# Optimization experiments

Measured on AMD Instinct MI355X. Metric: run time of the kernel, lower is better.

The kernel has to match this reference:

```python
import jax, jax.numpy as jnp
import numpy as np

B, N, EMB = 8, 1024, 768
HEADS = 8
INNER = EMB // HEADS          # 96: qkv inner dim (per the module's unusual design)
HEAD_D = INNER // HEADS       # 12: per-head dim after 'b n (h d) -> b h n d'
MLP = 3072
EPS = 1e-5


def _layernorm(x, g, b):
    mu = jnp.mean(x, axis=-1, keepdims=True)
    var = jnp.mean(jnp.square(x - mu), axis=-1, keepdims=True)
    return (x - mu) * jax.lax.rsqrt(var + EPS) * g + b


def setup_inputs() -> dict:
    key = jax.random.key(0)
    ks = jax.random.split(key, 8)
    s = 0.02
    return {
        "inputs": jax.random.normal(ks[0], (B, N, EMB), jnp.float32),
        "behaviors": jax.random.normal(ks[1], (B, 3), jnp.float32),
        "mouse_id": 0,
        "ln1_g": jnp.ones((EMB,), jnp.float32),
        "ln1_b": jnp.zeros((EMB,), jnp.float32),
        "w_qkv": jax.random.normal(ks[2], (EMB, 3 * INNER), jnp.float32) * s,
        "w_proj": jax.random.normal(ks[3], (INNER, EMB), jnp.float32) * s,
        "b_proj": jnp.zeros((EMB,), jnp.float32),
        "ln2_g": jnp.ones((EMB,), jnp.float32),
        "ln2_b": jnp.zeros((EMB,), jnp.float32),
        "w1": jax.random.normal(ks[4], (EMB, MLP), jnp.float32) * s,
        "b1": jnp.zeros((MLP,), jnp.float32),
        "w2": jax.random.normal(ks[5], (MLP, EMB), jnp.float32) * s,
        "b2": jnp.zeros((EMB,), jnp.float32),
    }


def reference(inputs, behaviors, mouse_id, ln1_g, ln1_b, w_qkv, w_proj, b_proj,
              ln2_g, ln2_b, w1, b1, w2, b2):
    # behavior_mode=0 -> b_mlp is None; dropout/drop_path = 0 -> identity.
    x = inputs
    # --- Attention (pre-LN) ---
    h = _layernorm(x, ln1_g, ln1_b)
    qkv = h @ w_qkv                                   # [B, N, 3*INNER]
    q, k, v = jnp.split(qkv, 3, axis=-1)
    def split_heads(a):
        return a.reshape(B, N, HEADS, HEAD_D)         # b n h d
    q = split_heads(q) * (INNER ** -0.5)              # scale = inner_dim^-0.5 (as in source)
    k = split_heads(k)
    v = split_heads(v)
    attn = jax.nn.softmax(jnp.einsum("bihd,bjhd->bhij", q, k), axis=-1)
    out = jnp.einsum("bhij,bjhd->bihd", attn, v).reshape(B, N, INNER)
    x = x + (out @ w_proj + b_proj)
    # --- MLP (pre-LN) ---
    m = _layernorm(x, ln2_g, ln2_b)
    m = jax.nn.gelu(m @ w1 + b1, approximate=False)   # nn.GELU default = exact erf
    x = x + (m @ w2 + b2)
    return x
```

## Files before the change

### kernel.cpp

```cpp
#include <hip/hip_runtime.h>
#include <hip/hip_bf16.h>
#include <math.h>

#define BB 8
#define NSEQ 1024
#define EMB 768
#define HEADS 8
#define INNER 96
#define HEAD_D 12
#define MLP_DIM 3072
#define ROWS (BB * NSEQ)

using short8  = __attribute__((ext_vector_type(8))) short;
using s4b     = __attribute__((ext_vector_type(4))) short;
using floatx4 = __attribute__((ext_vector_type(4))) float;

#define GLL16(g, l)                                                          \
    __builtin_amdgcn_global_load_lds(                                        \
        (const __attribute__((address_space(1))) void*)(g),                  \
        (__attribute__((address_space(3))) void*)(l), 16, 0, 0)

static __device__ __forceinline__ ushort f2b(float x) {
    __hip_bfloat16 h = __float2bfloat16(x);
    return *reinterpret_cast<ushort*>(&h);
}
static __device__ __forceinline__ uint pk2(float a, float b) {
    return (uint)f2b(a) | ((uint)f2b(b) << 16);
}

static __device__ __forceinline__ floatx4 mfma16(s4b a, s4b b, floatx4 c) {
#if __has_builtin(__builtin_amdgcn_mfma_f32_16x16x16_bf16)
    return __builtin_amdgcn_mfma_f32_16x16x16_bf16(a, b, c, 0, 0, 0);
#elif __has_builtin(__builtin_amdgcn_mfma_f32_16x16x16bf16_1k)
    return __builtin_amdgcn_mfma_f32_16x16x16bf16_1k(a, b, c, 0, 0, 0);
#else
    floatx4 d;
    asm("v_mfma_f32_16x16x16_bf16 %0, %1, %2, %3" : "=v"(d) : "v"(a), "v"(b), "v"(c));
    return d;
#endif
}

__global__ __launch_bounds__(256) void ln_bf16_kernel(const float* __restrict__ x,
                                                      const float* __restrict__ g,
                                                      const float* __restrict__ b,
                                                      ushort* __restrict__ out) {
    int row  = blockIdx.x * 4 + (threadIdx.x >> 6);
    int lane = threadIdx.x & 63;
    const float* xr = x + (size_t)row * EMB;
    float v[12];
    float s = 0.f;
#pragma unroll
    for (int i = 0; i < 12; i++) {
        v[i] = xr[lane + i * 64];
        s += v[i];
    }
#pragma unroll
    for (int off = 32; off; off >>= 1) s += __shfl_xor(s, off);
    float mu = s * (1.0f / EMB);
    float ss = 0.f;
#pragma unroll
    for (int i = 0; i < 12; i++) { float d = v[i] - mu; ss += d * d; }
#pragma unroll
    for (int off = 32; off; off >>= 1) ss += __shfl_xor(ss, off);
    float rstd = rsqrtf(ss * (1.0f / EMB) + 1e-5f);
    ushort* orow = out + (size_t)row * EMB;
#pragma unroll
    for (int i = 0; i < 12; i++) {
        int c = lane + i * 64;
        orow[c] = f2b((v[i] - mu) * rstd * g[c] + b[c]);
    }
}

__global__ __launch_bounds__(256) void convt_kernel(const float* __restrict__ in,
                                                    ushort* __restrict__ out,
                                                    int K, int N, int Npad) {
    __shared__ float t[32][33];
    int n0 = blockIdx.x * 32, k0 = blockIdx.y * 32;
    int tx = threadIdx.x, ty = threadIdx.y;
#pragma unroll
    for (int i = 0; i < 32; i += 8) {
        int n = n0 + tx;
        t[ty + i][tx] = (n < N) ? in[(size_t)(k0 + ty + i) * N + n] : 0.f;
    }
    __syncthreads();
#pragma unroll
    for (int i = 0; i < 32; i += 8) {
        out[(size_t)(n0 + ty + i) * K + k0 + tx] = f2b(t[tx][ty + i]);
    }
}

__global__ __launch_bounds__(256) void convt_pad_kernel(const float* __restrict__ in,
                                                        ushort* __restrict__ out,
                                                        int K, int N, int Kpad) {
    __shared__ float t[32][33];
    int n0 = blockIdx.x * 32, k0 = blockIdx.y * 32;
    int tx = threadIdx.x, ty = threadIdx.y;
#pragma unroll
    for (int i = 0; i < 32; i += 8) {
        int k = k0 + ty + i;
        t[ty + i][tx] = (k < K) ? in[(size_t)k * N + n0 + tx] : 0.f;
    }
    __syncthreads();
#pragma unroll
    for (int i = 0; i < 32; i += 8) {
        out[(size_t)(n0 + ty + i) * Kpad + k0 + tx] = f2b(t[tx][ty + i]);
    }
}

template <int EPI, bool MASKN>
__global__ __launch_bounds__(256) void gemm_mfma(const ushort* __restrict__ A,
                                                 const ushort* __restrict__ Bt,
                                                 void* __restrict__ Cout,
                                                 const float* __restrict__ bias,
                                                 const float* __restrict__ res,
                                                 int M, int Nn, int K, int gx) {
    __shared__ ushort As[2][128 * 64];
    __shared__ ushort Bs[2][128 * 64];
    int tid  = threadIdx.x;
    int lane = tid & 63, wave = tid >> 6;
    int wm = wave >> 1, wn = wave & 1;

    int nwg = gridDim.x;
    int lin = blockIdx.x;
    int swz = (lin & 7) * (nwg >> 3) + (lin >> 3);
    int by = swz / gx, bx = swz - by * gx;
    int m0 = by * 128, n0 = bx * 128;

    floatx4 acc[4][4] = {};

    int srow = lane >> 3;
    int slot = lane & 7;
    int nt = K >> 6;

    auto STAGE = [&](int t, int bufi) {
        int k0 = t << 6;
#pragma unroll
        for (int r = 0; r < 4; r++) {
            int row = r * 32 + wave * 8 + srow;
            int c   = slot ^ (row & 7);
            const ushort* ga = A  + (size_t)(m0 + row) * K + k0 + c * 8;
            const ushort* gb = Bt + (size_t)(n0 + row) * K + k0 + c * 8;
            GLL16(ga, (char*)&As[bufi][0] + r * 4096 + wave * 1024);
            GLL16(gb, (char*)&Bs[bufi][0] + r * 4096 + wave * 1024);
        }
    };

    STAGE(0, 0);
    STAGE(1, 1);
    asm volatile("s_waitcnt vmcnt(8)" ::: "memory");
    __builtin_amdgcn_s_barrier();
    __builtin_amdgcn_sched_barrier(0);

    int cur = 0;
    for (int t = 0; t < nt; ++t) {
        short8 af[2][4], bfr[2][4];
#pragma unroll
        for (int ks = 0; ks < 2; ks++) {
#pragma unroll
            for (int mi = 0; mi < 4; mi++) {
                int row = wm * 64 + mi * 16 + (lane & 15);
                int c   = ks * 4 + (lane >> 4);
                af[ks][mi] = *(const short8*)(&As[cur][0] + row * 64 + (c ^ (row & 7)) * 8);
            }
#pragma unroll
            for (int ni = 0; ni < 4; ni++) {
                int col = wn * 64 + ni * 16 + (lane & 15);
                int c   = ks * 4 + (lane >> 4);
                bfr[ks][ni] = *(const short8*)(&Bs[cur][0] + col * 64 + (c ^ (col & 7)) * 8);
            }
        }
        asm volatile("s_waitcnt lgkmcnt(0)" ::: "memory");
        __builtin_amdgcn_s_barrier();
        __builtin_amdgcn_sched_barrier(0);

        int tn = t + 2; if (tn > nt - 1) tn = nt - 1;
        STAGE(tn, cur);

        asm volatile("s_waitcnt vmcnt(8)" ::: "memory");
        __builtin_amdgcn_sched_barrier(0);

#pragma unroll
        for (int ks = 0; ks < 2; ks++)
#pragma unroll
            for (int mi = 0; mi < 4; mi++)
#pragma unroll
                for (int ni = 0; ni < 4; ni++)
                    acc[mi][ni] = __builtin_amdgcn_mfma_f32_16x16x32_bf16(
                        af[ks][mi], bfr[ks][ni], acc[mi][ni], 0, 0, 0);

        __builtin_amdgcn_s_barrier();
        __builtin_amdgcn_sched_barrier(0);
        cur ^= 1;
    }

    int r0 = m0 + wm * 64 + (lane >> 4) * 4;
    int c0 = n0 + wn * 64 + (lane & 15);
#pragma unroll
    for (int mi = 0; mi < 4; mi++) {
#pragma unroll
        for (int ni = 0; ni < 4; ni++) {
            int col = c0 + ni * 16;
            if (MASKN && col >= Nn) continue;
#pragma unroll
            for (int r = 0; r < 4; r++) {
                int row = r0 + mi * 16 + r;
                size_t idx = (size_t)row * Nn + col;
                float v = acc[mi][ni][r];
                if constexpr (EPI == 0) {
                    ((float*)Cout)[idx] = v;
                } else if constexpr (EPI == 1) {
                    ((float*)Cout)[idx] = v + bias[col] + res[idx];
                } else {
                    v += bias[col];
                    float u = v * (1.0f + 0.044715f * v * v);
                    float gl = v / (1.0f + __expf(-1.5957691216057308f * u));
                    ((ushort*)Cout)[idx] = f2b(gl);
                }
            }
        }
    }
}

__global__ __launch_bounds__(256) void attn_mfma_kernel(const float* __restrict__ qkv,
                                                        ushort* __restrict__ ao) {
    __shared__ ushort Kt[NSEQ * 12];
    __shared__ ushort VT[12 * 1032];
    int bh = blockIdx.x >> 3, qg = blockIdx.x & 7;
    int b = bh >> 3, h = bh & 7;
    int tid = threadIdx.x;
    const float* base = qkv + (size_t)b * NSEQ * (3 * INNER);

#pragma unroll
    for (int i = 0; i < 4; i++) {
        int j = i * 256 + tid;
        const float* kp = base + (size_t)j * (3 * INNER) + INNER + h * HEAD_D;
        float4 a0 = *(const float4*)(kp);
        float4 a1 = *(const float4*)(kp + 4);
        float4 a2 = *(const float4*)(kp + 8);
        uint2* kw = (uint2*)(&Kt[j * 12]);
        kw[0] = make_uint2(pk2(a0.x, a0.y), pk2(a0.z, a0.w));
        kw[1] = make_uint2(pk2(a1.x, a1.y), pk2(a1.z, a1.w));
        kw[2] = make_uint2(pk2(a2.x, a2.y), pk2(a2.z, a2.w));
        const float* vp = kp + INNER;
        float4 v0 = *(const float4*)(vp);
        float4 v1 = *(const float4*)(vp + 4);
        float4 v2 = *(const float4*)(vp + 8);
        VT[0 * 1032 + j] = f2b(v0.x);  VT[1 * 1032 + j]  = f2b(v0.y);
        VT[2 * 1032 + j] = f2b(v0.z);  VT[3 * 1032 + j]  = f2b(v0.w);
        VT[4 * 1032 + j] = f2b(v1.x);  VT[5 * 1032 + j]  = f2b(v1.y);
        VT[6 * 1032 + j] = f2b(v1.z);  VT[7 * 1032 + j]  = f2b(v1.w);
        VT[8 * 1032 + j] = f2b(v2.x);  VT[9 * 1032 + j]  = f2b(v2.y);
        VT[10 * 1032 + j] = f2b(v2.z); VT[11 * 1032 + j] = f2b(v2.w);
    }
    __syncthreads();

    int lane = tid & 63, wave = tid >> 6;
    int qrow = lane & 15, grp = lane >> 4;
    const float scale = 0.102062072615966f;

    s4b qf[2];
#pragma unroll
    for (int t = 0; t < 2; t++) {
        qf[t] = (s4b)0;
        if (grp < 3) {
            int q = qg * 128 + (wave * 2 + t) * 16 + qrow;
            const float* qp = base + (size_t)q * (3 * INNER) + h * HEAD_D + grp * 4;
            float4 qv = *(const float4*)(qp);
            uint2 u = make_uint2(pk2(qv.x * scale, qv.y * scale),
                                 pk2(qv.z * scale, qv.w * scale));
            qf[t] = __builtin_bit_cast(s4b, u);
        }
    }

    floatx4 acc[2] = {};
    float l[2] = {0.f, 0.f};
    int kc = (grp < 3) ? grp : 0;
    int dv = (qrow < 12) ? qrow : 0;
    bool kz = (grp == 3), vz = (qrow >= 12);
    const floatx4 z4 = {};

    for (int jt = 0; jt < 64; jt++) {
        s4b kf = *(const s4b*)(&Kt[(jt * 16 + qrow) * 12 + kc * 4]);
        if (kz) kf = (s4b)0;
        s4b vf = *(const s4b*)(&VT[dv * 1032 + jt * 16 + grp * 4]);
        if (vz) vf = (s4b)0;
#pragma unroll
        for (int t = 0; t < 2; t++) {
            floatx4 st = mfma16(kf, qf[t], z4);
            float p0 = __expf(st[0]), p1 = __expf(st[1]);
            float p2 = __expf(st[2]), p3 = __expf(st[3]);
            l[t] += (p0 + p1) + (p2 + p3);
            uint2 u = make_uint2(pk2(p0, p1), pk2(p2, p3));
            acc[t] = mfma16(vf, __builtin_bit_cast(s4b, u), acc[t]);
        }
    }

#pragma unroll
    for (int t = 0; t < 2; t++) {
        float lt = l[t];
        lt += __shfl_xor(lt, 16);
        lt += __shfl_xor(lt, 32);
        float inv = 1.f / lt;
        if (grp < 3) {
            int q = qg * 128 + (wave * 2 + t) * 16 + qrow;
            ushort4 o;
            o.x = f2b(acc[t][0] * inv);
            o.y = f2b(acc[t][1] * inv);
            o.z = f2b(acc[t][2] * inv);
            o.w = f2b(acc[t][3] * inv);
            *reinterpret_cast<ushort4*>(&ao[(size_t)(b * NSEQ + q) * 128 + h * HEAD_D + grp * 4]) = o;
        }
    }
}

extern "C" void kernel_launch(void* const* d_in, const int* in_sizes, int n_in,
                              void* d_out, int out_size, void* d_ws, size_t ws_size,
                              hipStream_t stream) {
    const float* inputs = (const float*)d_in[0];
    const float* ln1_g  = (const float*)d_in[3];
    const float* ln1_b  = (const float*)d_in[4];
    const float* w_qkv  = (const float*)d_in[5];
    const float* w_proj = (const float*)d_in[6];
    const float* b_proj = (const float*)d_in[7];
    const float* ln2_g  = (const float*)d_in[8];
    const float* ln2_b  = (const float*)d_in[9];
    const float* w1     = (const float*)d_in[10];
    const float* b1     = (const float*)d_in[11];
    const float* w2     = (const float*)d_in[12];
    const float* b2     = (const float*)d_in[13];
    float* out = (float*)d_out;

    char* ws = (char*)d_ws;
    ushort* h_bf    = (ushort*)(ws);
    float*  qkv     = (float*)(ws + 12582912);
    ushort* ao_pad  = (ushort*)(ws + 22020096);
    ushort* wproj_t = (ushort*)(ws + 24117248);
    float*  x1      = (float*)(ws + 25165824);
    ushort* m2      = (ushort*)(ws + 50331648);
    ushort* wqkv_t  = (ushort*)(ws + 100663296);
    ushort* w1_t    = (ushort*)(ws + 101253120);
    ushort* w2_t    = (ushort*)(ws + 105971712);

    dim3 tb(32, 8);
    convt_kernel<<<dim3(12, 24), tb, 0, stream>>>(w_qkv, wqkv_t, EMB, 3 * INNER, 384);
    convt_kernel<<<dim3(96, 24), tb, 0, stream>>>(w1, w1_t, EMB, MLP_DIM, MLP_DIM);
    convt_kernel<<<dim3(24, 96), tb, 0, stream>>>(w2, w2_t, MLP_DIM, EMB, EMB);
    convt_pad_kernel<<<dim3(24, 4), tb, 0, stream>>>(w_proj, wproj_t, INNER, EMB, 128);

    ln_bf16_kernel<<<ROWS / 4, 256, 0, stream>>>(inputs, ln1_g, ln1_b, h_bf);
    gemm_mfma<0, true><<<3 * (ROWS / 128), 256, 0, stream>>>(
        h_bf, wqkv_t, qkv, nullptr, nullptr, ROWS, 3 * INNER, EMB, 3);
    hipMemsetAsync(ao_pad, 0, (size_t)ROWS * 128 * 2, stream);
    attn_mfma_kernel<<<512, 256, 0, stream>>>(qkv, ao_pad);
    gemm_mfma<1, false><<<6 * (ROWS / 128), 256, 0, stream>>>(
        ao_pad, wproj_t, x1, b_proj, inputs, ROWS, EMB, 128, 6);
    ln_bf16_kernel<<<ROWS / 4, 256, 0, stream>>>(x1, ln2_g, ln2_b, h_bf);
    gemm_mfma<2, false><<<24 * (ROWS / 128), 256, 0, stream>>>(
        h_bf, w1_t, m2, b1, nullptr, ROWS, MLP_DIM, EMB, 24);
    gemm_mfma<1, false><<<6 * (ROWS / 128), 256, 0, stream>>>(
        m2, w2_t, out, b2, x1, ROWS, EMB, MLP_DIM, 6);
}
```

Measured before the change: 192.5 us.

## Use 256x128 tiles with 8 waves and triple-buffered LDS pipeline in GEMM

Replaces the 4-wave 128x128 double-buffered GEMM with an 8-wave 256x128 tile kernel that uses three LDS stages. Global-to-LDS loads for tile t+2 are split across two half-steps so they interleave with the MFMA bursts, and s_setprio is raised around those bursts. LDS addresses are precomputed once outside the loop. The aim is better latency hiding and more B-tile reuse per block. The cost is higher LDS use per block (about 144KB), which limits occupancy, and fewer blocks for the small-N GEMMs; the QKV GEMM launches only 96 blocks.

```diff
diff --git a/kernel.cpp b/kernel.cpp
--- a/kernel.cpp
+++ b/kernel.cpp
@@ -39,6 +39,7 @@
     return d;
 #endif
 }
+#define MFMA32(a, b, c) __builtin_amdgcn_mfma_f32_16x16x32_bf16((a), (b), (c), 0, 0, 0)
 
 __global__ __launch_bounds__(256) void ln_bf16_kernel(const float* __restrict__ x,
                                                       const float* __restrict__ g,
@@ -108,93 +109,155 @@
 }
 
 template <int EPI, bool MASKN>
-__global__ __launch_bounds__(256) void gemm_mfma(const ushort* __restrict__ A,
-                                                 const ushort* __restrict__ Bt,
-                                                 void* __restrict__ Cout,
-                                                 const float* __restrict__ bias,
-                                                 const float* __restrict__ res,
-                                                 int M, int Nn, int K, int gx) {
-    __shared__ ushort As[2][128 * 64];
-    __shared__ ushort Bs[2][128 * 64];
-    int tid  = threadIdx.x;
-    int lane = tid & 63, wave = tid >> 6;
-    int wm = wave >> 1, wn = wave & 1;
-
-    int nwg = gridDim.x;
-    int lin = blockIdx.x;
+__global__ __launch_bounds__(512) void gemm_mfma8(const ushort* __restrict__ A,
+                                                  const ushort* __restrict__ Bt,
+                                                  void* __restrict__ Cout,
+                                                  const float* __restrict__ bias,
+                                                  const float* __restrict__ res,
+                                                  int M, int Nn, int K, int gx) {
+    __shared__ ushort As3[3][256 * 64];
+    __shared__ ushort Bs3[3][128 * 64];
+    int tid = threadIdx.x, lane = tid & 63, w = tid >> 6;
+    int wm = w >> 1, wn = w & 1;
+
+    int nwg = gridDim.x, lin = blockIdx.x;
     int swz = (lin & 7) * (nwg >> 3) + (lin >> 3);
     int by = swz / gx, bx = swz - by * gx;
-    int m0 = by * 128, n0 = bx * 128;
+    int m0 = by * 256, n0 = bx * 128;
+    int nt = K >> 6;
+
+    int srow = lane >> 3;
+    int kchunk = (lane & 7) ^ srow;
+    const ushort* gA[4];
+    const ushort* gB[2];
+    uint loAB[4];
+#pragma unroll
+    for (int s = 0; s < 4; s++) {
+        int r = s * 64 + w * 8 + srow;
+        gA[s] = A + (size_t)(m0 + r) * K + kchunk * 8;
+        loAB[s] = (uint)(s * 512 + w * 64) * 16;
+    }
+#pragma unroll
+    for (int s = 0; s < 2; s++) {
+        int r = s * 64 + w * 8 + srow;
+        gB[s] = Bt + (size_t)(n0 + r) * K + kchunk * 8;
+    }
+#define STG_A(s_, buf_, kt_) GLL16(gA[s_] + (kt_) * 64, (char*)&As3[buf_][0] + loAB[s_])
+#define STG_B(s_, buf_, kt_) GLL16(gB[s_] + (kt_) * 64, (char*)&Bs3[buf_][0] + loAB[s_])
+
+    int qr = lane & 15, grp = lane >> 4;
+    uint aoff[2][4], boff[2][4];
+#pragma unroll
+    for (int ks = 0; ks < 2; ks++) {
+#pragma unroll
+        for (int mi = 0; mi < 4; mi++) {
+            int r = wm * 64 + mi * 16 + qr;
+            aoff[ks][mi] = (uint)(r * 64 + (((ks * 4 + grp) ^ (r & 7)) * 8));
+        }
+#pragma unroll
+        for (int ni = 0; ni < 4; ni++) {
+            int c = wn * 64 + ni * 16 + qr;
+            boff[ks][ni] = (uint)(c * 64 + (((ks * 4 + grp) ^ (c & 7)) * 8));
+        }
+    }
+
+    STG_A(0, 0, 0); STG_A(1, 0, 0); STG_A(2, 0, 0); STG_A(3, 0, 0);
+    STG_B(0, 0, 0); STG_B(1, 0, 0);
+    STG_A(0, 1, 1); STG_A(1, 1, 1); STG_A(2, 1, 1); STG_A(3, 1, 1);
+    STG_B(0, 1, 1); STG_B(1, 1, 1);
+    asm volatile("s_waitcnt vmcnt(6)" ::: "memory");
+    __builtin_amdgcn_sched_barrier(0);
+    __builtin_amdgcn_s_barrier();
 
     floatx4 acc[4][4] = {};
 
-    int srow = lane >> 3;
-    int slot = lane & 7;
-    int nt = K >> 6;
-
-    auto STAGE = [&](int t, int bufi) {
-        int k0 = t << 6;
-#pragma unroll
-        for (int r = 0; r < 4; r++) {
-            int row = r * 32 + wave * 8 + srow;
-            int c   = slot ^ (row & 7);
-            const ushort* ga = A  + (size_t)(m0 + row) * K + k0 + c * 8;
-            const ushort* gb = Bt + (size_t)(n0 + row) * K + k0 + c * 8;
-            GLL16(ga, (char*)&As[bufi][0] + r * 4096 + wave * 1024);
-            GLL16(gb, (char*)&Bs[bufi][0] + r * 4096 + wave * 1024);
-        }
-    };
-
-    STAGE(0, 0);
-    STAGE(1, 1);
-    asm volatile("s_waitcnt vmcnt(8)" ::: "memory");
-    __builtin_amdgcn_s_barrier();
-    __builtin_amdgcn_sched_barrier(0);
-
-    int cur = 0;
     for (int t = 0; t < nt; ++t) {
-        short8 af[2][4], bfr[2][4];
-#pragma unroll
-        for (int ks = 0; ks < 2; ks++) {
-#pragma unroll
-            for (int mi = 0; mi < 4; mi++) {
-                int row = wm * 64 + mi * 16 + (lane & 15);
-                int c   = ks * 4 + (lane >> 4);
-                af[ks][mi] = *(const short8*)(&As[cur][0] + row * 64 + (c ^ (row & 7)) * 8);
+        int buf = t % 3;
+        int nbuf = buf + 2; if (nbuf >= 3) nbuf -= 3;
+        const ushort* Ab = &As3[buf][0];
+        const ushort* Bb = &Bs3[buf][0];
+        bool st = (t + 2) < nt;
+        int t2 = t + 2;
+
+        {
+            short8 av0 = *(const short8*)(Ab + aoff[0][0]);
+            short8 av1 = *(const short8*)(Ab + aoff[0][1]);
+            short8 av2 = *(const short8*)(Ab + aoff[0][2]);
+            short8 av3 = *(const short8*)(Ab + aoff[0][3]);
+            short8 bv0 = *(const short8*)(Bb + boff[0][0]);
+            short8 bv1 = *(const short8*)(Bb + boff[0][1]);
+            short8 bv2 = *(const short8*)(Bb + boff[0][2]);
+            short8 bv3 = *(const short8*)(Bb + boff[0][3]);
+            if (st) { STG_A(0, nbuf, t2); STG_A(1, nbuf, t2); STG_A(2, nbuf, t2); }
+            __builtin_amdgcn_s_barrier();
+            asm volatile("s_waitcnt lgkmcnt(0)" ::: "memory");
+            __builtin_amdgcn_sched_barrier(0);
+            __builtin_amdgcn_s_setprio(1);
+            acc[0][0] = MFMA32(av0, bv0, acc[0][0]);
+            acc[0][1] = MFMA32(av0, bv1, acc[0][1]);
+            acc[0][2] = MFMA32(av0, bv2, acc[0][2]);
+            acc[0][3] = MFMA32(av0, bv3, acc[0][3]);
+            acc[1][0] = MFMA32(av1, bv0, acc[1][0]);
+            acc[1][1] = MFMA32(av1, bv1, acc[1][1]);
+            acc[1][2] = MFMA32(av1, bv2, acc[1][2]);
+            acc[1][3] = MFMA32(av1, bv3, acc[1][3]);
+            acc[2][0] = MFMA32(av2, bv0, acc[2][0]);
+            acc[2][1] = MFMA32(av2, bv1, acc[2][1]);
+            acc[2][2] = MFMA32(av2, bv2, acc[2][2]);
+            acc[2][3] = MFMA32(av2, bv3, acc[2][3]);
+            acc[3][0] = MFMA32(av3, bv0, acc[3][0]);
+            acc[3][1] = MFMA32(av3, bv1, acc[3][1]);
+            acc[3][2] = MFMA32(av3, bv2, acc[3][2]);
+            acc[3][3] = MFMA32(av3, bv3, acc[3][3]);
+            __builtin_amdgcn_s_setprio(0);
+            __builtin_amdgcn_sched_barrier(0);
+            __builtin_amdgcn_s_barrier();
+        }
+        {
+            short8 av0 = *(const short8*)(Ab + aoff[1][0]);
+            short8 av1 = *(const short8*)(Ab + aoff[1][1]);
+            short8 av2 = *(const short8*)(Ab + aoff[1][2]);
+            short8 av3 = *(const short8*)(Ab + aoff[1][3]);
+            short8 bv0 = *(const short8*)(Bb + boff[1][0]);
+            short8 bv1 = *(const short8*)(Bb + boff[1][1]);
+            short8 bv2 = *(const short8*)(Bb + boff[1][2]);
+            short8 bv3 = *(const short8*)(Bb + boff[1][3]);
+            if (st) { STG_A(3, nbuf, t2); STG_B(0, nbuf, t2); STG_B(1, nbuf, t2); }
+            __builtin_amdgcn_s_barrier();
+            asm volatile("s_waitcnt lgkmcnt(0)" ::: "memory");
+            __builtin_amdgcn_sched_barrier(0);
+            __builtin_amdgcn_s_setprio(1);
+            acc[0][0] = MFMA32(av0, bv0, acc[0][0]);
+            acc[0][1] = MFMA32(av0, bv1, acc[0][1]);
+            acc[0][2] = MFMA32(av0, bv2, acc[0][2]);
+            acc[0][3] = MFMA32(av0, bv3, acc[0][3]);
+            acc[1][0] = MFMA32(av1, bv0, acc[1][0]);
+            acc[1][1] = MFMA32(av1, bv1, acc[1][1]);
+            acc[1][2] = MFMA32(av1, bv2, acc[1][2]);
+            acc[1][3] = MFMA32(av1, bv3, acc[1][3]);
+            acc[2][0] = MFMA32(av2, bv0, acc[2][0]);
+            acc[2][1] = MFMA32(av2, bv1, acc[2][1]);
+            acc[2][2] = MFMA32(av2, bv2, acc[2][2]);
+            acc[2][3] = MFMA32(av2, bv3, acc[2][3]);
+            acc[3][0] = MFMA32(av3, bv0, acc[3][0]);
+            acc[3][1] = MFMA32(av3, bv1, acc[3][1]);
+            acc[3][2] = MFMA32(av3, bv2, acc[3][2]);
+            acc[3][3] = MFMA32(av3, bv3, acc[3][3]);
+            __builtin_amdgcn_s_setprio(0);
+            __builtin_amdgcn_sched_barrier(0);
+            if (t < nt - 1) {
+                if (st) asm volatile("s_waitcnt vmcnt(6)" ::: "memory");
+                else    asm volatile("s_waitcnt vmcnt(0)" ::: "memory");
+                __builtin_amdgcn_sched_barrier(0);
             }
-#pragma unroll
-            for (int ni = 0; ni < 4; ni++) {
-                int col = wn * 64 + ni * 16 + (lane & 15);
-                int c   = ks * 4 + (lane >> 4);
-                bfr[ks][ni] = *(const short8*)(&Bs[cur][0] + col * 64 + (c ^ (col & 7)) * 8);
-            }
-        }
-        asm volatile("s_waitcnt lgkmcnt(0)" ::: "memory");
-        __builtin_amdgcn_s_barrier();
-        __builtin_amdgcn_sched_barrier(0);
-
-        int tn = t + 2; if (tn > nt - 1) tn = nt - 1;
-        STAGE(tn, cur);
-
-        asm volatile("s_waitcnt vmcnt(8)" ::: "memory");
-        __builtin_amdgcn_sched_barrier(0);
-
-#pragma unroll
-        for (int ks = 0; ks < 2; ks++)
-#pragma unroll
-            for (int mi = 0; mi < 4; mi++)
-#pragma unroll
-                for (int ni = 0; ni < 4; ni++)
-                    acc[mi][ni] = __builtin_amdgcn_mfma_f32_16x16x32_bf16(
-                        af[ks][mi], bfr[ks][ni], acc[mi][ni], 0, 0, 0);
-
-        __builtin_amdgcn_s_barrier();
-        __builtin_amdgcn_sched_barrier(0);
-        cur ^= 1;
-    }
-
-    int r0 = m0 + wm * 64 + (lane >> 4) * 4;
-    int c0 = n0 + wn * 64 + (lane & 15);
+            __builtin_amdgcn_s_barrier();
+        }
+    }
+#undef STG_A
+#undef STG_B
+
+    int r0 = m0 + wm * 64 + grp * 4;
+    int c0 = n0 + wn * 64 + qr;
 #pragma unroll
     for (int mi = 0; mi < 4; mi++) {
 #pragma unroll
@@ -348,15 +411,15 @@
     convt_pad_kernel<<<dim3(24, 4), tb, 0, stream>>>(w_proj, wproj_t, INNER, EMB, 128);
 
     ln_bf16_kernel<<<ROWS / 4, 256, 0, stream>>>(inputs, ln1_g, ln1_b, h_bf);
-    gemm_mfma<0, true><<<3 * (ROWS / 128), 256, 0, stream>>>(
+    gemm_mfma8<0, true><<<96, 512, 0, stream>>>(
         h_bf, wqkv_t, qkv, nullptr, nullptr, ROWS, 3 * INNER, EMB, 3);
     hipMemsetAsync(ao_pad, 0, (size_t)ROWS * 128 * 2, stream);
     attn_mfma_kernel<<<512, 256, 0, stream>>>(qkv, ao_pad);
-    gemm_mfma<1, false><<<6 * (ROWS / 128), 256, 0, stream>>>(
+    gemm_mfma8<1, false><<<192, 512, 0, stream>>>(
         ao_pad, wproj_t, x1, b_proj, inputs, ROWS, EMB, 128, 6);
     ln_bf16_kernel<<<ROWS / 4, 256, 0, stream>>>(x1, ln2_g, ln2_b, h_bf);
-    gemm_mfma<2, false><<<24 * (ROWS / 128), 256, 0, stream>>>(
+    gemm_mfma8<2, false><<<768, 512, 0, stream>>>(
         h_bf, w1_t, m2, b1, nullptr, ROWS, MLP_DIM, EMB, 24);
-    gemm_mfma<1, false><<<6 * (ROWS / 128), 256, 0, stream>>>(
+    gemm_mfma8<1, false><<<192, 512, 0, stream>>>(
         m2, w2_t, out, b2, x1, ROWS, EMB, MLP_DIM, 6);
 }
```

After: 211.4 us. 9.8% more time.

## Overlap LDS fragment loads with MFMA by splitting k-steps and raising priority

Applied to the files above, without the earlier changes.

Restructures the GEMM main loop so the first k-half's MFMAs start once its LDS fragments arrive (lgkmcnt(8)), while the second half's fragments are still in flight. The second k-half's MFMAs now run after the barrier and next-tile staging, overlapping global loads. It also precomputes swizzled LDS offsets outside the loop and raises wave priority around MFMA blocks with s_setprio. The aim is to hide LDS and global latency behind matrix work. The cost is more live registers and a more order-sensitive schedule.

```diff
diff --git a/kernel.cpp b/kernel.cpp
--- a/kernel.cpp
+++ b/kernel.cpp
@@ -39,6 +39,7 @@
     return d;
 #endif
 }
+#define MFMA32(a, b, c) __builtin_amdgcn_mfma_f32_16x16x32_bf16((a), (b), (c), 0, 0, 0)
 
 __global__ __launch_bounds__(256) void ln_bf16_kernel(const float* __restrict__ x,
                                                       const float* __restrict__ g,
@@ -145,56 +146,75 @@
         }
     };
 
+    int qr = lane & 15, grp = lane >> 4;
+    uint aoff[2][4], boff[2][4];
+#pragma unroll
+    for (int ks = 0; ks < 2; ks++) {
+#pragma unroll
+        for (int mi = 0; mi < 4; mi++) {
+            int r = wm * 64 + mi * 16 + qr;
+            aoff[ks][mi] = (uint)(r * 64 + (((ks * 4 + grp) ^ (r & 7)) * 8));
+        }
+#pragma unroll
+        for (int ni = 0; ni < 4; ni++) {
+            int c = wn * 64 + ni * 16 + qr;
+            boff[ks][ni] = (uint)(c * 64 + (((ks * 4 + grp) ^ (c & 7)) * 8));
+        }
+    }
+
     STAGE(0, 0);
     STAGE(1, 1);
     asm volatile("s_waitcnt vmcnt(8)" ::: "memory");
+    __builtin_amdgcn_sched_barrier(0);
     __builtin_amdgcn_s_barrier();
-    __builtin_amdgcn_sched_barrier(0);
 
     int cur = 0;
     for (int t = 0; t < nt; ++t) {
-        short8 af[2][4], bfr[2][4];
-#pragma unroll
-        for (int ks = 0; ks < 2; ks++) {
-#pragma unroll
-            for (int mi = 0; mi < 4; mi++) {
-                int row = wm * 64 + mi * 16 + (lane & 15);
-                int c   = ks * 4 + (lane >> 4);
-                af[ks][mi] = *(const short8*)(&As[cur][0] + row * 64 + (c ^ (row & 7)) * 8);
-            }
-#pragma unroll
-            for (int ni = 0; ni < 4; ni++) {
-                int col = wn * 64 + ni * 16 + (lane & 15);
-                int c   = ks * 4 + (lane >> 4);
-                bfr[ks][ni] = *(const short8*)(&Bs[cur][0] + col * 64 + (c ^ (col & 7)) * 8);
-            }
-        }
+        const ushort* Ab = &As[cur][0];
+        const ushort* Bb = &Bs[cur][0];
+        short8 a0[4], b0[4], a1[4], b1[4];
+#pragma unroll
+        for (int mi = 0; mi < 4; mi++) a0[mi] = *(const short8*)(Ab + aoff[0][mi]);
+#pragma unroll
+        for (int ni = 0; ni < 4; ni++) b0[ni] = *(const short8*)(Bb + boff[0][ni]);
+#pragma unroll
+        for (int mi = 0; mi < 4; mi++) a1[mi] = *(const short8*)(Ab + aoff[1][mi]);
+#pragma unroll
+        for (int ni = 0; ni < 4; ni++) b1[ni] = *(const short8*)(Bb + boff[1][ni]);
+
+        asm volatile("s_waitcnt lgkmcnt(8)" ::: "memory");
+        __builtin_amdgcn_sched_barrier(0);
+        __builtin_amdgcn_s_setprio(1);
+#pragma unroll
+        for (int mi = 0; mi < 4; mi++)
+#pragma unroll
+            for (int ni = 0; ni < 4; ni++)
+                acc[mi][ni] = MFMA32(a0[mi], b0[ni], acc[mi][ni]);
+        __builtin_amdgcn_s_setprio(0);
+
         asm volatile("s_waitcnt lgkmcnt(0)" ::: "memory");
+        __builtin_amdgcn_sched_barrier(0);
         __builtin_amdgcn_s_barrier();
-        __builtin_amdgcn_sched_barrier(0);
 
         int tn = t + 2; if (tn > nt - 1) tn = nt - 1;
         STAGE(tn, cur);
 
+        __builtin_amdgcn_s_setprio(1);
+#pragma unroll
+        for (int mi = 0; mi < 4; mi++)
+#pragma unroll
+            for (int ni = 0; ni < 4; ni++)
+                acc[mi][ni] = MFMA32(a1[mi], b1[ni], acc[mi][ni]);
+        __builtin_amdgcn_s_setprio(0);
+
         asm volatile("s_waitcnt vmcnt(8)" ::: "memory");
         __builtin_amdgcn_sched_barrier(0);
-
-#pragma unroll
-        for (int ks = 0; ks < 2; ks++)
-#pragma unroll
-            for (int mi = 0; mi < 4; mi++)
-#pragma unroll
-                for (int ni = 0; ni < 4; ni++)
-                    acc[mi][ni] = __builtin_amdgcn_mfma_f32_16x16x32_bf16(
-                        af[ks][mi], bfr[ks][ni], acc[mi][ni], 0, 0, 0);
-
         __builtin_amdgcn_s_barrier();
-        __builtin_amdgcn_sched_barrier(0);
         cur ^= 1;
     }
 
-    int r0 = m0 + wm * 64 + (lane >> 4) * 4;
-    int c0 = n0 + wn * 64 + (lane & 15);
+    int r0 = m0 + wm * 64 + grp * 4;
+    int c0 = n0 + wn * 64 + qr;
 #pragma unroll
     for (int mi = 0; mi < 4; mi++) {
 #pragma unroll
```

After: 199.7 us. +3.7%, slower.

## Add 256x256-tile 8-wave GEMM kernel for the MLP up-projection

Applied to the files above, without the earlier changes.

Adds a new GEMM kernel with 256x256 output tiles, 512 threads (8 waves in a 2x4 grid, each computing 128x64), and double-buffered direct-to-LDS loads with an XOR-swizzled layout. The kernel is used for the w1 GEMM with fused bias+GELU, replacing the 128x128 tile kernel (384 blocks instead of 1536). The intent is to raise arithmetic intensity and reuse of A/B tiles per global load. In exchange it uses 128KB of LDS and many more accumulator registers per thread, which limits occupancy to one block per CU, and the grid is only 384 blocks.

```diff
diff --git a/kernel.cpp b/kernel.cpp
--- a/kernel.cpp
+++ b/kernel.cpp
@@ -38,6 +38,12 @@
     asm("v_mfma_f32_16x16x16_bf16 %0, %1, %2, %3" : "=v"(d) : "v"(a), "v"(b), "v"(c));
     return d;
 #endif
+}
+#define MFMA32(a, b, c) __builtin_amdgcn_mfma_f32_16x16x32_bf16((a), (b), (c), 0, 0, 0)
+
+static __device__ __forceinline__ float gelu_f(float v) {
+    float u = v * (1.0f + 0.044715f * v * v);
+    return v / (1.0f + __expf(-1.5957691216057308f * u));
 }
 
 __global__ __launch_bounds__(256) void ln_bf16_kernel(const float* __restrict__ x,
@@ -148,8 +154,8 @@
     STAGE(0, 0);
     STAGE(1, 1);
     asm volatile("s_waitcnt vmcnt(8)" ::: "memory");
+    __builtin_amdgcn_sched_barrier(0);
     __builtin_amdgcn_s_barrier();
-    __builtin_amdgcn_sched_barrier(0);
 
     int cur = 0;
     for (int t = 0; t < nt; ++t) {
@@ -185,16 +191,16 @@
             for (int mi = 0; mi < 4; mi++)
 #pragma unroll
                 for (int ni = 0; ni < 4; ni++)
-                    acc[mi][ni] = __builtin_amdgcn_mfma_f32_16x16x32_bf16(
-                        af[ks][mi], bfr[ks][ni], acc[mi][ni], 0, 0, 0);
+                    acc[mi][ni] = MFMA32(af[ks][mi], bfr[ks][ni], acc[mi][ni]);
 
         __builtin_amdgcn_s_barrier();
         __builtin_amdgcn_sched_barrier(0);
         cur ^= 1;
     }
 
-    int r0 = m0 + wm * 64 + (lane >> 4) * 4;
-    int c0 = n0 + wn * 64 + (lane & 15);
+    int qr = lane & 15, grp = lane >> 4;
+    int r0 = m0 + wm * 64 + grp * 4;
+    int c0 = n0 + wn * 64 + qr;
 #pragma unroll
     for (int mi = 0; mi < 4; mi++) {
 #pragma unroll
@@ -211,10 +217,117 @@
                 } else if constexpr (EPI == 1) {
                     ((float*)Cout)[idx] = v + bias[col] + res[idx];
                 } else {
-                    v += bias[col];
-                    float u = v * (1.0f + 0.044715f * v * v);
-                    float gl = v / (1.0f + __expf(-1.5957691216057308f * u));
-                    ((ushort*)Cout)[idx] = f2b(gl);
+                    ((ushort*)Cout)[idx] = f2b(gelu_f(v + bias[col]));
+                }
+            }
+        }
+    }
+}
+
+template <int EPI>
+__global__ __launch_bounds__(512) void gemm_mfma256(const ushort* __restrict__ A,
+                                                    const ushort* __restrict__ Bt,
+                                                    void* __restrict__ Cout,
+                                                    const float* __restrict__ bias,
+                                                    const float* __restrict__ res,
+                                                    int M, int Nn, int K, int gx) {
+    __shared__ ushort As[2][256 * 64];
+    __shared__ ushort Bs[2][256 * 64];
+    int tid = threadIdx.x, lane = tid & 63, w = tid >> 6;
+    int wm = w >> 2, wn = w & 3;
+
+    int nwg = gridDim.x, lin = blockIdx.x;
+    int swz = (lin & 7) * (nwg >> 3) + (lin >> 3);
+    int by = swz / gx, bx = swz - by * gx;
+    int m0 = by * 256, n0 = bx * 256;
+    int nt = K >> 6;
+
+    int srow = lane >> 3, slot = lane & 7;
+
+    auto STAGE = [&](int t, int bufi) {
+        int k0 = t << 6;
+#pragma unroll
+        for (int r = 0; r < 4; r++) {
+            int row = r * 64 + w * 8 + srow;
+            int c   = slot ^ (row & 7);
+            const ushort* ga = A  + (size_t)(m0 + row) * K + k0 + c * 8;
+            const ushort* gb = Bt + (size_t)(n0 + row) * K + k0 + c * 8;
+            GLL16(ga, (char*)&As[bufi][0] + r * 8192 + w * 1024);
+            GLL16(gb, (char*)&Bs[bufi][0] + r * 8192 + w * 1024);
+        }
+    };
+
+    int qr = lane & 15, grp = lane >> 4;
+
+    STAGE(0, 0);
+    STAGE(1, 1);
+    asm volatile("s_waitcnt vmcnt(8)" ::: "memory");
+    __builtin_amdgcn_sched_barrier(0);
+    __builtin_amdgcn_s_barrier();
+
+    floatx4 acc[8][4] = {};
+
+    int cur = 0;
+    for (int t = 0; t < nt; ++t) {
+        const ushort* Ab = &As[cur][0];
+        const ushort* Bb = &Bs[cur][0];
+        short8 af[2][8], bfr[2][4];
+#pragma unroll
+        for (int ks = 0; ks < 2; ks++) {
+#pragma unroll
+            for (int mi = 0; mi < 8; mi++) {
+                int row = wm * 128 + mi * 16 + qr;
+                int c   = ks * 4 + grp;
+                af[ks][mi] = *(const short8*)(Ab + row * 64 + ((c ^ (row & 7)) * 8));
+            }
+#pragma unroll
+            for (int ni = 0; ni < 4; ni++) {
+                int col = wn * 64 + ni * 16 + qr;
+                int c   = ks * 4 + grp;
+                bfr[ks][ni] = *(const short8*)(Bb + col * 64 + ((c ^ (col & 7)) * 8));
+            }
+        }
+        asm volatile("s_waitcnt lgkmcnt(0)" ::: "memory");
+        __builtin_amdgcn_s_barrier();
+        __builtin_amdgcn_sched_barrier(0);
+
+        int tn = t + 2; if (tn > nt - 1) tn = nt - 1;
+        STAGE(tn, cur);
+
+        asm volatile("s_waitcnt vmcnt(8)" ::: "memory");
+        __builtin_amdgcn_sched_barrier(0);
+
+#pragma unroll
+        for (int ks = 0; ks < 2; ks++)
+#pragma unroll
+            for (int mi = 0; mi < 8; mi++)
+#pragma unroll
+                for (int ni = 0; ni < 4; ni++)
+                    acc[mi][ni] = MFMA32(af[ks][mi], bfr[ks][ni], acc[mi][ni]);
+
+        __builtin_amdgcn_s_barrier();
+        __builtin_amdgcn_sched_barrier(0);
+        cur ^= 1;
+    }
+
+    int r0 = m0 + wm * 128 + grp * 4;
+    int c0 = n0 + wn * 64 + qr;
+#pragma unroll
+    for (int mi = 0; mi < 8; mi++) {
+#pragma unroll
+        for (int ni = 0; ni < 4; ni++) {
+            int col = c0 + ni * 16;
+#pragma unroll
+            for (int r = 0; r < 4; r++) {
+                int row = r0 + mi * 16 + r;
+                size_t idx = (size_t)row * Nn + col;
+                float v = acc[mi][ni][r];
+                if constexpr (EPI == 0) {
+                    ((float*)Cout)[idx] = v;
+                } else if constexpr (EPI == 1) {
+                    ((float*)Cout)[idx] = v + bias[col] + res[idx];
+                } else {
+                    ((ushort*)Cout)[idx] = f2b(gelu_f(v + bias[col]));
                 }
             }
         }
@@ -355,8 +468,8 @@
     gemm_mfma<1, false><<<6 * (ROWS / 128), 256, 0, stream>>>(
         ao_pad, wproj_t, x1, b_proj, inputs, ROWS, EMB, 128, 6);
     ln_bf16_kernel<<<ROWS / 4, 256, 0, stream>>>(x1, ln2_g, ln2_b, h_bf);
-    gemm_mfma<2, false><<<24 * (ROWS / 128), 256, 0, stream>>>(
-        h_bf, w1_t, m2, b1, nullptr, ROWS, MLP_DIM, EMB, 24);
+    gemm_mfma256<2><<<384, 512, 0, stream>>>(
+        h_bf, w1_t, m2, b1, nullptr, ROWS, MLP_DIM, EMB, 12);
     gemm_mfma<1, false><<<6 * (ROWS / 128), 256, 0, stream>>>(
         m2, w2_t, out, b2, x1, ROWS, EMB, MLP_DIM, 6);
 }
```

New measurement: 200.8 us. +4.3%, slower.
